# Kernel optimization log

Measured on AMD Instinct MI355X. Metric: run time of the kernel, lower is better.

Reference implementation:

```python
import jax, jax.numpy as jnp
import numpy as np
from functools import partial

GRID = 5  # 224/32 - 2
N_ANCHORS = 3
N_BOX = GRID * GRID * N_ANCHORS  # 75


def _make_anchors():
    # faithful replication of _create_anchors (grid-index cx,cy with pixel-scale w,h)
    scales = [56, 112, 224]
    a = np.zeros((GRID, GRID, N_ANCHORS, 8), np.float32)
    for x in range(GRID):
        for y in range(GRID):
            for k in range(N_ANCHORS):
                w = h = scales[k]
                a[x, y, k] = [x - w // 2, y - h // 2, x + w // 2, y + h // 2, x, y, w, h]
    return jnp.asarray(a)

ANCHORS = _make_anchors()  # [5,5,3,8]: x0,y0,x1,y1,cx,cy,w,h


def conv2d(x, w, b, pad):
    y = jax.lax.conv_general_dilated(x, w, (1, 1), [(pad, pad), (pad, pad)],
                                     dimension_numbers=('NCHW', 'OIHW', 'NCHW'))
    return y + b[None, :, None, None]


def maxpool2(x):
    return jax.lax.reduce_window(x, -jnp.inf, jax.lax.max,
                                 (1, 1, 2, 2), (1, 1, 2, 2), 'VALID')


def deparam_bboxes(rp_reg):
    # rp_reg: [B,5,5,3,4]; anchors broadcast over batch
    aw = ANCHORS[..., 6]; ah = ANCHORS[..., 7]
    ax = ANCHORS[..., 4]; ay = ANCHORS[..., 5]
    cx = rp_reg[..., 0] * aw + ax
    cy = rp_reg[..., 1] * ah + ay
    w = jnp.exp(rp_reg[..., 2]) * aw
    h = jnp.exp(rp_reg[..., 3]) * ah
    return jnp.stack([cx - w / 2, cy - h / 2, cx + w / 2, cy + h / 2], axis=-1)


def _iou_as_written(bi, bj):
    # replicates bb_intersection_over_union EXACTLY, including the missing
    # parentheses bug: inter/areaA + areaB - inter
    xA = jnp.maximum(bi[0], bj[..., 0]); yA = jnp.maximum(bi[1], bj[..., 1])
    xB = jnp.minimum(bi[2], bj[..., 2]); yB = jnp.minimum(bi[3], bj[..., 3])
    inter = jnp.maximum(0.0, xB - xA + 1) * jnp.maximum(0.0, yB - yA + 1)
    areaA = (bi[2] - bi[0] + 1) * (bi[3] - bi[1] + 1)
    areaB = (bj[..., 2] - bj[..., 0] + 1) * (bj[..., 3] - bj[..., 1] + 1)
    return inter / areaA + areaB - inter


def nms_single(boxes, scores, thresh=0.7):
    # boxes [75,4], scores [75]; greedy suppression in score order (vectorized
    # replacement of the O(n^2) Python-loop NMS in _compute_bboxes)
    order = jnp.argsort(-scores)
    b = boxes[order]
    idx = jnp.arange(N_BOX)

    def body(i, keep):
        iou = _iou_as_written(b[i], b)          # [75]
        sup = (idx > i) & (iou > thresh) & keep[i]
        return keep & ~sup

    keep_sorted = jax.lax.fori_loop(0, N_BOX, body, jnp.ones(N_BOX, bool))
    return jnp.zeros(N_BOX, bool).at[order].set(keep_sorted)


def setup_inputs() -> dict:
    key = jax.random.key(0)
    ks = jax.random.split(key, 16)
    B = 32
    inp = {"x": jax.random.normal(ks[0], (B, 3, 224, 224), jnp.float32)}
    chans = [3, 64, 128, 256, 512, 512]
    for i in range(5):
        cin, cout = chans[i], chans[i + 1]
        std = float(np.sqrt(2.0 / (cout * 9)))  # kaiming fan_out, relu
        inp[f"fw{i}"] = jax.random.normal(ks[1 + i], (cout, cin, 3, 3), jnp.float32) * std
        inp[f"fb{i}"] = jnp.zeros((cout,), jnp.float32)
    # RPN heads: normal(0, 0.01), zero bias (per _initialize_rp_weights)
    inp["rpw_w"] = jax.random.normal(ks[6], (512, 512, 3, 3), jnp.float32) * 0.01
    inp["rpw_b"] = jnp.zeros((512,), jnp.float32)
    inp["cls_w"] = jax.random.normal(ks[7], (N_ANCHORS, 512, 1, 1), jnp.float32) * 0.01
    inp["cls_b"] = jnp.zeros((N_ANCHORS,), jnp.float32)
    inp["reg_w"] = jax.random.normal(ks[8], (4 * N_ANCHORS, 512, 1, 1), jnp.float32) * 0.01
    inp["reg_b"] = jnp.zeros((4 * N_ANCHORS,), jnp.float32)
    # classifier2: Linear(512*7*7, 20), normal(0, 0.01)
    inp["fc_w"] = jax.random.normal(ks[9], (20, 512 * 7 * 7), jnp.float32) * 0.01
    inp["fc_b"] = jnp.zeros((20,), jnp.float32)
    return inp


def reference(x, fw0, fb0, fw1, fb1, fw2, fb2, fw3, fb3, fw4, fb4,
              rpw_w, rpw_b, cls_w, cls_b, reg_w, reg_b, fc_w, fc_b):
    B = x.shape[0]
    feat = x
    for w, b in ((fw0, fb0), (fw1, fb1), (fw2, fb2), (fw3, fb3), (fw4, fb4)):
        feat = maxpool2(jax.nn.relu(conv2d(feat, w, b, pad=1)))
    # feat: [B,512,7,7]
    rp512 = jax.nn.relu(conv2d(feat, rpw_w, rpw_b, pad=0))          # [B,512,5,5]
    rp_cls = jax.nn.sigmoid(conv2d(rp512, cls_w, cls_b, pad=0))     # [B,3,5,5]
    rp_reg = conv2d(rp512, reg_w, reg_b, pad=0)                     # [B,12,5,5]
    # faithful to torch .view (row-major reshape, NOT permute)
    rp_cls = rp_cls.reshape(B, GRID, GRID, N_ANCHORS)
    rp_reg = rp_reg.reshape(B, GRID, GRID, N_ANCHORS, 4)
    bboxes = deparam_bboxes(rp_reg)                                 # [B,5,5,3,4]
    keep = jax.vmap(nms_single)(bboxes.reshape(B, N_BOX, 4),
                                rp_cls.reshape(B, N_BOX))           # [B,75] bool
    logits = feat.reshape(B, -1) @ fc_w.T + fc_b                    # [B,20]
    return logits, rp_cls, rp_reg, bboxes, keep
```

## Files before the change

### kernel.cpp

```cpp
#include <hip/hip_runtime.h>
#include <math.h>


#define OFF_LOGITS 0
#define OFF_CLS    640
#define OFF_REG    3040
#define OFF_BOXES  12640
#define OFF_KEEP   22240

constexpr int BATCH = 32;

typedef _Float16 h8 __attribute__((ext_vector_type(8)));
typedef _Float16 h4 __attribute__((ext_vector_type(4)));
typedef float    f4 __attribute__((ext_vector_type(4)));

#define MFMA16(a, b, c) __builtin_amdgcn_mfma_f32_16x16x32_f16(a, b, c, 0, 0, 0)

#if defined(__has_builtin)
#  if __has_builtin(__builtin_amdgcn_global_load_lds)
#    define HAS_GLL 1
#  endif
#endif

__device__ __forceinline__ void stage16(const _Float16* g, _Float16* lbase, int lane) {
#ifdef HAS_GLL
  __builtin_amdgcn_global_load_lds((const __attribute__((address_space(1))) void*)g,
                                   (__attribute__((address_space(3))) void*)lbase,
                                   16, 0, 0);
#else
  *reinterpret_cast<h8*>(lbase + lane * 8) = *reinterpret_cast<const h8*>(g);
#endif
}

constexpr size_t A_OFF = 0;
constexpr size_t B_OFF = 106463232;
constexpr size_t W_OFF = 161579008;
constexpr size_t P_OFF = A_OFF + 8388608;

constexpr int I0_E = 26615808;
constexpr int I1_E = 13778944;
constexpr int I2_E = 7372800;
constexpr int I3_E = 4194304;
constexpr int I4_E = 802816;

__global__ __launch_bounds__(256)
void wcvt(const float* __restrict__ src, _Float16* __restrict__ dHi,
          _Float16* __restrict__ dLo, int COUT, int CIN) {
  const int total = COUT * CIN * 9;
  for (int idx = blockIdx.x * 256 + threadIdx.x; idx < total; idx += gridDim.x * 256) {
    const int co = idx / (CIN * 9);
    const int r = idx % (CIN * 9);
    const int ci = r / 9, tap = r % 9;
    const float v = src[idx];
    const _Float16 h = (_Float16)v;
    const int o = ((tap * (CIN >> 5) + (ci >> 5)) * COUT + co) * 32 + (ci & 31);
    dHi[o] = h;
    dLo[o] = (_Float16)(v - (float)h);
  }
}

__global__ __launch_bounds__(256)
void zero_ring(_Float16* __restrict__ hi, _Float16* __restrict__ lo, int P, int C) {
  const int c8n = C / 8, cells = 4 * P - 4;
  const int tot = 32 * cells * c8n;
  for (int idx = blockIdx.x * 256 + threadIdx.x; idx < tot; idx += gridDim.x * 256) {
    const int c8 = idx % c8n;
    const int cell = (idx / c8n) % cells;
    const int n = idx / (c8n * cells);
    int y, xx;
    if (cell < 2 * P) { y = (cell < P) ? 0 : (P - 1); xx = cell % P; }
    else { const int q = cell - 2 * P; y = 1 + (q >> 1); xx = (q & 1) ? (P - 1) : 0; }
    const long o = ((long)(n * P + y) * P + xx) * C + c8 * 8;
    h8 z = {};
    *reinterpret_cast<h8*>(hi + o) = z;
    *reinterpret_cast<h8*>(lo + o) = z;
  }
}

__global__ __launch_bounds__(256)
void conv_l0(const float* __restrict__ x, const float* __restrict__ w0,
             const float* __restrict__ b0, _Float16* __restrict__ outHi,
             _Float16* __restrict__ outLo) {
  const int bid = blockIdx.x;
  const int tx0 = (bid % 7) * 16, ty0 = ((bid / 7) % 7) * 16, n = bid / 49;
  __shared__ float sIn[3 * 34 * 34];
  __shared__ float sW[1728];
  __shared__ float sB[64];
  const int tid = threadIdx.x;
  for (int idx = tid; idx < 3 * 34 * 34; idx += 256) {
    const int ci = idx / 1156, rem = idx % 1156, r = rem / 34, cc = rem % 34;
    const int y = 2 * ty0 - 1 + r, xx = 2 * tx0 - 1 + cc;
    float v = 0.f;
    if ((unsigned)y < 224u && (unsigned)xx < 224u)
      v = x[((n * 3 + ci) * 224 + y) * 224 + xx];
    sIn[idx] = v;
  }
  for (int idx = tid; idx < 1728; idx += 256) sW[idx] = w0[idx];
  if (tid < 64) sB[tid] = b0[tid];
  __syncthreads();

  const int tpy = tid / 16, tpx = tid % 16;
  float win[3][4][4];
  #pragma unroll
  for (int ci = 0; ci < 3; ++ci)
    #pragma unroll
    for (int dr = 0; dr < 4; ++dr)
      #pragma unroll
      for (int dc = 0; dc < 4; ++dc)
        win[ci][dr][dc] = sIn[ci * 1156 + (2 * tpy + dr) * 34 + (2 * tpx + dc)];

  const long ob = ((long)(n * 114 + ty0 + tpy + 1) * 114 + tx0 + tpx + 1) * 64;
  for (int co4 = 0; co4 < 16; ++co4) {
    h4 hh, ll;
    #pragma unroll
    for (int j = 0; j < 4; ++j) {
      const int co = co4 * 4 + j;
      float a00 = 0.f, a01 = 0.f, a10 = 0.f, a11 = 0.f;
      #pragma unroll
      for (int ci = 0; ci < 3; ++ci)
        #pragma unroll
        for (int ky = 0; ky < 3; ++ky)
          #pragma unroll
          for (int kx = 0; kx < 3; ++kx) {
            const float wv = sW[co * 27 + ci * 9 + ky * 3 + kx];
            a00 = fmaf(win[ci][ky][kx], wv, a00);
            a01 = fmaf(win[ci][ky][kx + 1], wv, a01);
            a10 = fmaf(win[ci][ky + 1][kx], wv, a10);
            a11 = fmaf(win[ci][ky + 1][kx + 1], wv, a11);
          }
      const float p = fmaxf(fmaxf(fmaxf(a00, a01), fmaxf(a10, a11)) + sB[co], 0.f);
      const _Float16 h = (_Float16)p;
      hh[j] = h;
      ll[j] = (_Float16)(p - (float)h);
    }
    *reinterpret_cast<h4*>(outHi + ob + co4 * 4) = hh;
    *reinterpret_cast<h4*>(outLo + ob + co4 * 4) = ll;
  }
}

template<int CIN, int COUT, int H, int XPAD>
__global__ __launch_bounds__(256, 2)
void convrow(const _Float16* __restrict__ inHi, const _Float16* __restrict__ inLo,
             const _Float16* __restrict__ wHi, const _Float16* __restrict__ wLo,
             const float* __restrict__ bias, _Float16* __restrict__ outHi,
             _Float16* __restrict__ outLo) {
  constexpr int W = H, Hp = H / 2, Wp = W / 2, PW = W + 2, POW = Wp + 2;
  constexpr int BSP = XPAD * 2;
  constexpr int NSPW = BSP / 64;
  constexpr int NCOW = 4 / NSPW;
  constexpr int BCO = NCOW * 64;
  constexpr int KCH = CIN / 32;
  constexpr int NPH = 3 * KCH;
  constexpr int NISS = BSP / 64;
  __align__(16) __shared__ _Float16 sB[2][2][BSP * 32];

  const int tid = threadIdx.x;
  const int lane = tid & 63, wv = tid >> 6;
  const int c = lane & 15, kq = lane >> 4;
  const int cow = blockIdx.y * BCO + (wv % NCOW) * 64;
  const int spl = (wv / NCOW) * 64;
  const int py = blockIdx.x % Hp, n = blockIdx.x / Hp;

  int gstage[NISS];
  #pragma unroll
  for (int i = 0; i < NISS; ++i) {
    const int sl = i * 64 + tid / 4;
    const int ry = sl & 1;
    int xx = sl >> 1;
    if (xx > PW - 1) xx = PW - 1;
    gstage[i] = ((n * (H + 2) + 2 * py + ry) * PW + xx) * CIN +
                (((tid & 3) ^ ((sl >> 1) & 3)) * 8);
  }
  int dsoff[3][4];
  #pragma unroll
  for (int kx = 0; kx < 3; ++kx)
    #pragma unroll
    for (int nt = 0; nt < 4; ++nt) {
      int r = spl + nt * 16 + c + 2 * kx;
      if (r > BSP - 1) r = BSP - 1;
      dsoff[kx][nt] = r * 32 + ((kq ^ ((r >> 1) & 3)) * 8);
    }

  #pragma unroll
  for (int i = 0; i < NISS; ++i) {
    stage16(inHi + gstage[i], &sB[0][0][i * 2048 + wv * 512], lane);
    stage16(inLo + gstage[i], &sB[0][1][i * 2048 + wv * 512], lane);
  }
  __syncthreads();

  f4 acc[4][4] = {};
  int cur = 0;
  for (int ph = 0; ph < NPH; ++ph) {
    const int ky = ph / KCH, kc = ph % KCH;
    h8 aH[3][4], aL[3][4];
    #pragma unroll
    for (int kx = 0; kx < 3; ++kx) {
      const long abase = ((long)((ky * 3 + kx) * KCH + kc) * COUT + cow) * 32;
      #pragma unroll
      for (int mt = 0; mt < 4; ++mt) {
        const long ao = abase + (mt * 16 + c) * 32 + kq * 8;
        aH[kx][mt] = *reinterpret_cast<const h8*>(wHi + ao);
        aL[kx][mt] = *reinterpret_cast<const h8*>(wLo + ao);
      }
    }
    __builtin_amdgcn_sched_barrier(0);
    if (ph + 1 < NPH) {
      const int tb2 = ((ph + 1) / KCH) * PW * CIN + ((ph + 1) % KCH) * 32;
      #pragma unroll
      for (int i = 0; i < NISS; ++i) {
        stage16(inHi + gstage[i] + tb2, &sB[cur ^ 1][0][i * 2048 + wv * 512], lane);
        stage16(inLo + gstage[i] + tb2, &sB[cur ^ 1][1][i * 2048 + wv * 512], lane);
      }
    }
    __builtin_amdgcn_sched_barrier(0);
    #pragma unroll
    for (int kx = 0; kx < 3; ++kx) {
      h8 bH[4], bL[4];
      #pragma unroll
      for (int nt = 0; nt < 4; ++nt) {
        bH[nt] = *reinterpret_cast<const h8*>(&sB[cur][0][dsoff[kx][nt]]);
        bL[nt] = *reinterpret_cast<const h8*>(&sB[cur][1][dsoff[kx][nt]]);
      }
      __builtin_amdgcn_s_setprio(1);
      #pragma unroll
      for (int mt = 0; mt < 4; ++mt)
        #pragma unroll
        for (int nt = 0; nt < 4; ++nt)
          acc[mt][nt] = MFMA16(aH[kx][mt], bH[nt], acc[mt][nt]);
      #pragma unroll
      for (int mt = 0; mt < 4; ++mt)
        #pragma unroll
        for (int nt = 0; nt < 4; ++nt)
          acc[mt][nt] = MFMA16(aH[kx][mt], bL[nt], acc[mt][nt]);
      #pragma unroll
      for (int mt = 0; mt < 4; ++mt)
        #pragma unroll
        for (int nt = 0; nt < 4; ++nt)
          acc[mt][nt] = MFMA16(aL[kx][mt], bH[nt], acc[mt][nt]);
      __builtin_amdgcn_s_setprio(0);
    }
    __syncthreads();
    cur ^= 1;
  }

  const int r4 = lane >> 4;
  #pragma unroll
  for (int mt = 0; mt < 4; ++mt) {
    const int co0 = cow + mt * 16 + r4 * 4;
    const f4 bi = *reinterpret_cast<const f4*>(bias + co0);
    #pragma unroll
    for (int nt = 0; nt < 4; ++nt) {
      f4 v = acc[mt][nt];
      #pragma unroll
      for (int r = 0; r < 4; ++r) {
        const float m1 = fmaxf(v[r], __shfl_xor(v[r], 1, 64));
        v[r] = fmaxf(m1, __shfl_xor(m1, 2, 64));
      }
      if ((lane & 3) == 0) {
        const int rr = spl + nt * 16 + c;
        const int px = rr >> 2;
        if (px < Wp) {
          h4 hh, ll;
          #pragma unroll
          for (int r = 0; r < 4; ++r) {
            const float p = fmaxf(v[r] + bi[r], 0.f);
            const _Float16 h = (_Float16)p;
            hh[r] = h;
            ll[r] = (_Float16)(p - (float)h);
          }
          const long oa = ((long)((n * (Hp + 2) + py + 1) * POW + px + 1)) * COUT + co0;
          *reinterpret_cast<h4*>(outHi + oa) = hh;
          *reinterpret_cast<h4*>(outLo + oa) = ll;
        }
      }
    }
  }
}

template<int CIN, int COUT, int H, int BCO, int BSP, int TG, int KPH, int MODE>
__global__ __launch_bounds__(256, 2)
void convpool(const _Float16* __restrict__ inHi, const _Float16* __restrict__ inLo,
              const _Float16* __restrict__ wHi, const _Float16* __restrict__ wLo,
              const float* __restrict__ bias, _Float16* __restrict__ outHi,
              _Float16* __restrict__ outLo, float* __restrict__ outF) {
  constexpr int W = H, Hp = H / 2, Wp = W / 2, PW = W + 2, POW = Wp + 2;
  constexpr int NCOW = BCO / 64, NSPW = BSP / 64;
  static_assert(NCOW * NSPW == 4, "4 waves");
  constexpr int KCH = CIN / 32;
  constexpr int NCH = TG * KCH;
  constexpr int NPH = NCH / KPH;
  static_assert(NCH % KPH == 0, "even phases");
  constexpr int NISS = BSP / 64;
  constexpr int SPTOT = 32 * H * W;
  constexpr int TSZ = BSP * 32;
  __align__(16) __shared__ _Float16 sB[2 * 2 * KPH * TSZ];
  #define TIDX(buf, hl, j) ((((buf) * 2 + (hl)) * KPH + (j)) * TSZ)

  const int tid = threadIdx.x;
  const int lane = tid & 63, wv = tid >> 6;
  const int c = lane & 15, kq = lane >> 4;
  const int cow = blockIdx.y * BCO + (wv % NCOW) * 64;
  const int spl = (wv / NCOW) * 64;
  const int sblk = blockIdx.x * BSP;
  const int tap0 = (TG == 9) ? 0 : blockIdx.z * TG;

  int gstage[NISS];
  #pragma unroll
  for (int i = 0; i < NISS; ++i) {
    const int sl = i * 64 + tid / 4;
    const int sg = sblk + sl;
    const int ry = sg & 1, tt = sg >> 1;
    const int x = tt % W, u = tt / W;
    const int py = u % Hp, n = u / Hp;
    gstage[i] = ((n * (H + 2) + 2 * py + ry) * PW + x) * CIN +
                (((tid & 3) ^ ((sl >> 1) & 3)) * 8);
  }
  int dsoff[4];
  #pragma unroll
  for (int nt = 0; nt < 4; ++nt) {
    const int row = spl + nt * 16 + c;
    dsoff[nt] = row * 32 + ((kq ^ ((row >> 1) & 3)) * 8);
  }

  #pragma unroll
  for (int j = 0; j < KPH; ++j) {
    const int tap = tap0 + j / KCH, kc = j % KCH;
    const int tb = ((tap / 3) * PW + (tap % 3)) * CIN + kc * 32;
    #pragma unroll
    for (int i = 0; i < NISS; ++i) {
      stage16(inHi + gstage[i] + tb, &sB[TIDX(0, 0, j) + i * 2048 + wv * 512], lane);
      stage16(inLo + gstage[i] + tb, &sB[TIDX(0, 1, j) + i * 2048 + wv * 512], lane);
    }
  }
  __syncthreads();

  f4 acc[4][4] = {};
  int cur = 0;
  for (int ph = 0; ph < NPH; ++ph) {
    h8 aH[KPH][4], aL[KPH][4];
    #pragma unroll
    for (int j = 0; j < KPH; ++j) {
      const int ch = ph * KPH + j;
      const int tap = tap0 + ch / KCH;
      const int kc = ch % KCH;
      const long abase = ((long)(tap * KCH + kc) * COUT + cow) * 32;
      #pragma unroll
      for (int mt = 0; mt < 4; ++mt) {
        const long ao = abase + (mt * 16 + c) * 32 + kq * 8;
        aH[j][mt] = *reinterpret_cast<const h8*>(wHi + ao);
        aL[j][mt] = *reinterpret_cast<const h8*>(wLo + ao);
      }
    }
    __builtin_amdgcn_sched_barrier(0);
    if (ph + 1 < NPH) {
      #pragma unroll
      for (int j2 = 0; j2 < KPH; ++j2) {
        const int ch2 = (ph + 1) * KPH + j2;
        const int tap2 = tap0 + ch2 / KCH;
        const int tb2 = ((tap2 / 3) * PW + (tap2 % 3)) * CIN + (ch2 % KCH) * 32;
        #pragma unroll
        for (int i = 0; i < NISS; ++i) {
          stage16(inHi + gstage[i] + tb2,
                  &sB[TIDX(cur ^ 1, 0, j2) + i * 2048 + wv * 512], lane);
          stage16(inLo + gstage[i] + tb2,
                  &sB[TIDX(cur ^ 1, 1, j2) + i * 2048 + wv * 512], lane);
        }
      }
    }
    __builtin_amdgcn_sched_barrier(0);
    #pragma unroll
    for (int j = 0; j < KPH; ++j) {
      h8 bH[4], bL[4];
      #pragma unroll
      for (int nt = 0; nt < 4; ++nt) {
        bH[nt] = *reinterpret_cast<const h8*>(&sB[TIDX(cur, 0, j) + dsoff[nt]]);
        bL[nt] = *reinterpret_cast<const h8*>(&sB[TIDX(cur, 1, j) + dsoff[nt]]);
      }
      __builtin_amdgcn_s_setprio(1);
      #pragma unroll
      for (int mt = 0; mt < 4; ++mt)
        #pragma unroll
        for (int nt = 0; nt < 4; ++nt)
          acc[mt][nt] = MFMA16(aH[j][mt], bH[nt], acc[mt][nt]);
      #pragma unroll
      for (int mt = 0; mt < 4; ++mt)
        #pragma unroll
        for (int nt = 0; nt < 4; ++nt)
          acc[mt][nt] = MFMA16(aH[j][mt], bL[nt], acc[mt][nt]);
      #pragma unroll
      for (int mt = 0; mt < 4; ++mt)
        #pragma unroll
        for (int nt = 0; nt < 4; ++nt)
          acc[mt][nt] = MFMA16(aL[j][mt], bH[nt], acc[mt][nt]);
      __builtin_amdgcn_s_setprio(0);
    }
    __syncthreads();
    cur ^= 1;
  }
  #undef TIDX

  const int r4 = lane >> 4;
  if (MODE == 1) {
    #pragma unroll
    for (int mt = 0; mt < 4; ++mt) {
      const int co0 = cow + mt * 16 + r4 * 4;
      #pragma unroll
      for (int nt = 0; nt < 4; ++nt) {
        const int s = sblk + spl + nt * 16 + c;
        *reinterpret_cast<f4*>(outF + ((long)blockIdx.z * SPTOT + s) * COUT + co0) =
            acc[mt][nt];
      }
    }
  } else {
    #pragma unroll
    for (int mt = 0; mt < 4; ++mt) {
      const int co0 = cow + mt * 16 + r4 * 4;
      const f4 bi = *reinterpret_cast<const f4*>(bias + co0);
      #pragma unroll
      for (int nt = 0; nt < 4; ++nt) {
        f4 v = acc[mt][nt];
        #pragma unroll
        for (int r = 0; r < 4; ++r) {
          const float m1 = fmaxf(v[r], __shfl_xor(v[r], 1, 64));
          v[r] = fmaxf(m1, __shfl_xor(m1, 2, 64));
        }
        if ((lane & 3) == 0) {
          const int s = sblk + spl + nt * 16 + c;
          const int ps = s >> 2;
          const int n = ps / (Hp * Wp), rem = ps % (Hp * Wp);
          const int py = rem / Wp, px = rem % Wp;
          h4 hh, ll;
          #pragma unroll
          for (int r = 0; r < 4; ++r) {
            const float p = fmaxf(v[r] + bi[r], 0.f);
            const _Float16 h = (_Float16)p;
            hh[r] = h;
            ll[r] = (_Float16)(p - (float)h);
          }
          const long oa = ((long)((n * (Hp + 2) + py + 1) * POW + px + 1)) * COUT + co0;
          *reinterpret_cast<h4*>(outHi + oa) = hh;
          *reinterpret_cast<h4*>(outLo + oa) = ll;
        }
      }
    }
  }
}

__global__ __launch_bounds__(256)
void l4_finish(const float* __restrict__ part, const float* __restrict__ bias,
               _Float16* __restrict__ I4h, _Float16* __restrict__ I4l,
               float* __restrict__ feat) {
  const int t = blockIdx.x * 256 + threadIdx.x;
  if (t >= 1568 * 128) return;
  const int co0 = (t % 128) * 4, p = t / 128;
  f4 m;
  #pragma unroll
  for (int q = 0; q < 4; ++q) {
    const long s = 4L * p + q;
    f4 v = *reinterpret_cast<const f4*>(part + s * 512 + co0);
    v += *reinterpret_cast<const f4*>(part + (6272 + s) * 512 + co0);
    v += *reinterpret_cast<const f4*>(part + (12544 + s) * 512 + co0);
    if (q == 0) m = v;
    else {
      #pragma unroll
      for (int r = 0; r < 4; ++r) m[r] = fmaxf(m[r], v[r]);
    }
  }
  const f4 bi = *reinterpret_cast<const f4*>(bias + co0);
  h4 hh, ll;
  const int n = p / 49, pix = p % 49;
  #pragma unroll
  for (int r = 0; r < 4; ++r) {
    const float pv = fmaxf(m[r] + bi[r], 0.f);
    const _Float16 h = (_Float16)pv;
    hh[r] = h;
    ll[r] = (_Float16)(pv - (float)h);
    feat[((long)(n * 512 + co0 + r)) * 49 + pix] = pv;
  }
  *reinterpret_cast<h4*>(I4h + (long)p * 512 + co0) = hh;
  *reinterpret_cast<h4*>(I4l + (long)p * 512 + co0) = ll;
}

__global__ __launch_bounds__(256)
void rpn_partial(const _Float16* __restrict__ inHi, const _Float16* __restrict__ inLo,
                 const _Float16* __restrict__ wHi, const _Float16* __restrict__ wLo,
                 float* __restrict__ part) {
  const int lane = threadIdx.x & 63, wv = threadIdx.x >> 6;
  const int cow = blockIdx.y * 128 + wv * 32;
  const int sblk = blockIdx.x * 64;
  const int tap = blockIdx.z, ky = tap / 3, kx = tap % 3;
  const int c = lane & 15, kq = lane >> 4;

  int baseB[4];
  #pragma unroll
  for (int nt = 0; nt < 4; ++nt) {
    int s = sblk + nt * 16 + c;
    if (s > 799) s = 799;
    const int n = s / 25, pix = s % 25, py = pix / 5, px = pix % 5;
    baseB[nt] = ((n * 7 + py + ky) * 7 + px + kx) * 512;
  }

  f4 acc[2][4] = {};
  for (int kch = 0; kch < 16; ++kch) {
    h8 aH[2], aL[2], bH[4], bL[4];
    const long abase = ((long)(tap * 16 + kch) * 512 + cow) * 32;
    #pragma unroll
    for (int mt = 0; mt < 2; ++mt) {
      const long ao = abase + (mt * 16 + c) * 32 + kq * 8;
      aH[mt] = *reinterpret_cast<const h8*>(wHi + ao);
      aL[mt] = *reinterpret_cast<const h8*>(wLo + ao);
    }
    #pragma unroll
    for (int nt = 0; nt < 4; ++nt) {
      const int bo = baseB[nt] + kch * 32 + kq * 8;
      bH[nt] = *reinterpret_cast<const h8*>(inHi + bo);
      bL[nt] = *reinterpret_cast<const h8*>(inLo + bo);
    }
    #pragma unroll
    for (int mt = 0; mt < 2; ++mt)
      #pragma unroll
      for (int nt = 0; nt < 4; ++nt)
        acc[mt][nt] = MFMA16(aH[mt], bH[nt], acc[mt][nt]);
    #pragma unroll
    for (int mt = 0; mt < 2; ++mt)
      #pragma unroll
      for (int nt = 0; nt < 4; ++nt)
        acc[mt][nt] = MFMA16(aH[mt], bL[nt], acc[mt][nt]);
    #pragma unroll
    for (int mt = 0; mt < 2; ++mt)
      #pragma unroll
      for (int nt = 0; nt < 4; ++nt)
        acc[mt][nt] = MFMA16(aL[mt], bH[nt], acc[mt][nt]);
  }

  const int r4 = lane >> 4;
  #pragma unroll
  for (int mt = 0; mt < 2; ++mt) {
    const int co0 = cow + mt * 16 + r4 * 4;
    #pragma unroll
    for (int nt = 0; nt < 4; ++nt) {
      const int s = sblk + nt * 16 + c;
      if (s < 800)
        *reinterpret_cast<f4*>(part + ((long)tap * 800 + s) * 512 + co0) = acc[mt][nt];
    }
  }
}

__global__ __launch_bounds__(256)
void rpn_finish(const float* __restrict__ part, const float* __restrict__ bias,
                float* __restrict__ rp512) {
  const int t = blockIdx.x * 256 + threadIdx.x;
  if (t >= 800 * 128) return;
  const int co0 = (t % 128) * 4, s = t / 128;
  f4 acc = *reinterpret_cast<const f4*>(bias + co0);
  #pragma unroll
  for (int g = 0; g < 9; ++g)
    acc += *reinterpret_cast<const f4*>(part + ((long)g * 800 + s) * 512 + co0);
  f4 o;
  #pragma unroll
  for (int r = 0; r < 4; ++r) o[r] = fmaxf(acc[r], 0.f);
  *reinterpret_cast<f4*>(rp512 + (long)s * 512 + co0) = o;
}

__global__ __launch_bounds__(256)
void heads_kernel(const float* __restrict__ rp512,
                  const float* __restrict__ cls_w, const float* __restrict__ cls_b,
                  const float* __restrict__ reg_w, const float* __restrict__ reg_b,
                  float* __restrict__ out) {
  const int idx = blockIdx.x * 256 + threadIdx.x;
  if (idx >= 32 * 25 * 15) return;
  const int o = idx % 15, pix = (idx / 15) % 25, n = idx / 375;
  const float* __restrict__ ip = rp512 + ((long)(n * 25 + pix)) * 512;
  const float* __restrict__ wvp = (o < 3) ? (cls_w + o * 512) : (reg_w + (o - 3) * 512);
  float acc = 0.f;
  for (int k = 0; k < 512; k += 4) {
    const f4 a = *reinterpret_cast<const f4*>(ip + k);
    const f4 b = *reinterpret_cast<const f4*>(wvp + k);
    acc = fmaf(a[0], b[0], acc); acc = fmaf(a[1], b[1], acc);
    acc = fmaf(a[2], b[2], acc); acc = fmaf(a[3], b[3], acc);
  }
  if (o < 3) {
    acc += cls_b[o];
    out[OFF_CLS + n * 75 + o * 25 + pix] = 1.f / (1.f + expf(-acc));
  } else {
    acc += reg_b[o - 3];
    out[OFF_REG + n * 300 + (o - 3) * 25 + pix] = acc;
  }
}

__global__ __launch_bounds__(256)
void fc_kernel(const float* __restrict__ feat, const float* __restrict__ fw,
               const float* __restrict__ fb, float* __restrict__ out) {
  const int n = blockIdx.x, j = blockIdx.y;
  const float* __restrict__ ip = feat + (long)n * 25088;
  const float* __restrict__ wj = fw + (long)j * 25088;
  float acc = 0.f;
  for (int k = threadIdx.x * 4; k < 25088; k += 1024) {
    const f4 a = *reinterpret_cast<const f4*>(ip + k);
    const f4 b = *reinterpret_cast<const f4*>(wj + k);
    acc = fmaf(a[0], b[0], acc); acc = fmaf(a[1], b[1], acc);
    acc = fmaf(a[2], b[2], acc); acc = fmaf(a[3], b[3], acc);
  }
  #pragma unroll
  for (int m = 32; m >= 1; m >>= 1) acc += __shfl_xor(acc, m, 64);
  __shared__ float red[4];
  const int wv = threadIdx.x >> 6;
  if ((threadIdx.x & 63) == 0) red[wv] = acc;
  __syncthreads();
  if (threadIdx.x == 0)
    out[OFF_LOGITS + n * 20 + j] = red[0] + red[1] + red[2] + red[3] + fb[j];
}

__global__ __launch_bounds__(128)
void bbox_nms_kernel(float* __restrict__ out) {
  const int n = blockIdx.x;
  const int t = threadIdx.x;
  __shared__ float bx0[75], by0[75], bx1[75], by1[75], area[75], sc[75];
  __shared__ int rank_s[75], order_s[75], keep_s[75];

  if (t < 75) {
    const int g1 = t / 15, g2 = (t / 3) % 5, a = t % 3;
    const float aw = (a == 0) ? 56.f : (a == 1 ? 112.f : 224.f);
    const float r0 = out[OFF_REG + n * 300 + 4 * t + 0];
    const float r1 = out[OFF_REG + n * 300 + 4 * t + 1];
    const float r2 = out[OFF_REG + n * 300 + 4 * t + 2];
    const float r3 = out[OFF_REG + n * 300 + 4 * t + 3];
    const float cx = r0 * aw + (float)g1;
    const float cy = r1 * aw + (float)g2;
    const float w_ = expf(r2) * aw;
    const float h_ = expf(r3) * aw;
    const float x0 = cx - 0.5f * w_, y0 = cy - 0.5f * h_;
    const float x1 = cx + 0.5f * w_, y1 = cy + 0.5f * h_;
    bx0[t] = x0; by0[t] = y0; bx1[t] = x1; by1[t] = y1;
    area[t] = (x1 - x0 + 1.f) * (y1 - y0 + 1.f);
    out[OFF_BOXES + n * 300 + 4 * t + 0] = x0;
    out[OFF_BOXES + n * 300 + 4 * t + 1] = y0;
    out[OFF_BOXES + n * 300 + 4 * t + 2] = x1;
    out[OFF_BOXES + n * 300 + 4 * t + 3] = y1;
    sc[t] = out[OFF_CLS + n * 75 + t];
    keep_s[t] = 1;
  }
  __syncthreads();
  if (t < 75) {
    const float si = sc[t];
    int rk = 0;
    for (int j = 0; j < 75; ++j) {
      const float sj = sc[j];
      rk += (sj > si) || (sj == si && j < t);
    }
    rank_s[t] = rk;
    order_s[rk] = t;
  }
  __syncthreads();
  for (int i = 0; i < 74; ++i) {
    if (keep_s[i]) {
      const int bi = order_s[i];
      if (t > i && t < 75) {
        const int bj = order_s[t];
        const float xA = fmaxf(bx0[bi], bx0[bj]);
        const float yA = fmaxf(by0[bi], by0[bj]);
        const float xB = fminf(bx1[bi], bx1[bj]);
        const float yB = fminf(by1[bi], by1[bj]);
        const float inter = fmaxf(0.f, xB - xA + 1.f) * fmaxf(0.f, yB - yA + 1.f);
        const float iou = inter / area[bi] + area[bj] - inter;
        if (iou > 0.7f) keep_s[t] = 0;
      }
    }
    __syncthreads();
  }
  if (t < 75) out[OFF_KEEP + n * 75 + t] = keep_s[rank_s[t]] ? 1.f : 0.f;
}

extern "C" void kernel_launch(void* const* d_in, const int* in_sizes, int n_in,
                              void* d_out, int out_size, void* d_ws, size_t ws_size,
                              hipStream_t stream) {
  (void)in_sizes; (void)n_in; (void)out_size; (void)ws_size;
  const float* x     = (const float*)d_in[0];
  const float* fw0   = (const float*)d_in[1];
  const float* fb0   = (const float*)d_in[2];
  const float* fw1   = (const float*)d_in[3];
  const float* fb1   = (const float*)d_in[4];
  const float* fw2   = (const float*)d_in[5];
  const float* fb2   = (const float*)d_in[6];
  const float* fw3   = (const float*)d_in[7];
  const float* fb3   = (const float*)d_in[8];
  const float* fw4   = (const float*)d_in[9];
  const float* fb4   = (const float*)d_in[10];
  const float* rpw_w = (const float*)d_in[11];
  const float* rpw_b = (const float*)d_in[12];
  const float* cls_w = (const float*)d_in[13];
  const float* cls_b = (const float*)d_in[14];
  const float* reg_w = (const float*)d_in[15];
  const float* reg_b = (const float*)d_in[16];
  const float* fc_w  = (const float*)d_in[17];
  const float* fc_b  = (const float*)d_in[18];
  float* out = (float*)d_out;
  char* ws = (char*)d_ws;

  _Float16* I0h = (_Float16*)(ws + A_OFF);
  _Float16* I0l = I0h + I0_E;
  _Float16* I1h = (_Float16*)(ws + B_OFF);
  _Float16* I1l = I1h + I1_E;
  _Float16* I2h = (_Float16*)(ws + A_OFF);
  _Float16* I2l = I2h + I2_E;
  _Float16* I3h = (_Float16*)(ws + B_OFF);
  _Float16* I3l = I3h + I3_E;
  _Float16* I4h = (_Float16*)(ws + A_OFF);
  _Float16* I4l = I4h + I4_E;
  float* feat  = (float*)(ws + A_OFF + (size_t)I4_E * 4);
  float* rp512 = (float*)(ws + A_OFF + (size_t)I4_E * 4 + 3211264);
  float* part  = (float*)(ws + P_OFF);

  _Float16* w1h = (_Float16*)(ws + W_OFF);                _Float16* w1l = w1h + 73728;
  _Float16* w2h = (_Float16*)(ws + W_OFF + 294912);       _Float16* w2l = w2h + 294912;
  _Float16* w3h = (_Float16*)(ws + W_OFF + 1474560);      _Float16* w3l = w3h + 1179648;
  _Float16* w4h = (_Float16*)(ws + W_OFF + 6193152);      _Float16* w4l = w4h + 2359296;
  _Float16* wrh = (_Float16*)(ws + W_OFF + 15630336);     _Float16* wrl = wrh + 2359296;

  wcvt<<<(73728 + 255) / 256, 256, 0, stream>>>(fw1, w1h, w1l, 128, 64);
  wcvt<<<(294912 + 255) / 256, 256, 0, stream>>>(fw2, w2h, w2l, 256, 128);
  wcvt<<<(1179648 + 255) / 256, 256, 0, stream>>>(fw3, w3h, w3l, 512, 256);
  wcvt<<<(2359296 + 255) / 256, 256, 0, stream>>>(fw4, w4h, w4l, 512, 512);
  wcvt<<<(2359296 + 255) / 256, 256, 0, stream>>>(rpw_w, wrh, wrl, 512, 512);

  zero_ring<<<512, 256, 0, stream>>>(I0h, I0l, 114, 64);
  zero_ring<<<512, 256, 0, stream>>>(I1h, I1l, 58, 128);

  conv_l0<<<32 * 49, 256, 0, stream>>>(x, fw0, fb0, I0h, I0l);

  convrow<64, 128, 112, 128><<<dim3(32 * 56, 2), 256, 0, stream>>>(
      I0h, I0l, w1h, w1l, fb1, I1h, I1l);
  zero_ring<<<512, 256, 0, stream>>>(I2h, I2l, 30, 256);
  convrow<128, 256, 56, 64><<<dim3(32 * 28, 2), 256, 0, stream>>>(
      I1h, I1l, w2h, w2l, fb2, I2h, I2l);
  zero_ring<<<512, 256, 0, stream>>>(I3h, I3l, 16, 512);
  convrow<256, 512, 28, 32><<<dim3(32 * 14, 2), 256, 0, stream>>>(
      I2h, I2l, w3h, w3l, fb3, I3h, I3l);
  convpool<512, 512, 14, 256, 64, 3, 2, 1><<<dim3(98, 2, 3), 256, 0, stream>>>(
      I3h, I3l, w4h, w4l, nullptr, nullptr, nullptr, part);
  l4_finish<<<(1568 * 128 + 255) / 256, 256, 0, stream>>>(part, fb4, I4h, I4l, feat);

  rpn_partial<<<dim3(13, 4, 9), 256, 0, stream>>>(I4h, I4l, wrh, wrl, part);
  rpn_finish<<<(800 * 128 + 255) / 256, 256, 0, stream>>>(part, rpw_b, rp512);

  heads_kernel<<<(12000 + 255) / 256, 256, 0, stream>>>(rp512, cls_w, cls_b, reg_w, reg_b, out);
  fc_kernel<<<dim3(32, 20), 256, 0, stream>>>(feat, fc_w, fc_b, out);
  bbox_nms_kernel<<<BATCH, 128, 0, stream>>>(out);
}
```

Measured before the change: 1.023 ms.

## Retile conv layers, triple-buffer convpool staging, and coalesce layer-0 output stores

Layer 0 now stages its fp16 hi/lo outputs in shared memory and writes them back as 16-byte coalesced stores instead of strided 8-byte ones. Layer 1 moves to a new convrow2 that splits each output row into 64-pixel halves with a fixed 128-channel tile per block. Layers 2 and 3 switch from the row kernel to the convpool implicit-GEMM kernel. convpool moves from double to triple buffering: it prefetches two phases ahead, uses a partial vmcnt wait and raw s_barrier, and no longer waits for all loads each phase. The aim is more latency hiding and better grid occupancy, at the cost of more LDS per block and a fragile hand-written waitcnt assumption.

```diff
diff --git a/kernel.cpp b/kernel.cpp
--- a/kernel.cpp
+++ b/kernel.cpp
@@ -77,15 +77,23 @@
   }
 }
 
+constexpr int L0_SW   = 0;
+constexpr int L0_SB   = 6912;
+constexpr int L0_SIN  = 7168;
+constexpr int L0_HI   = 7168;
+constexpr int L0_LO   = 7168 + 36864;
+constexpr int L0_LDS  = 7168 + 73728;
+
 __global__ __launch_bounds__(256)
 void conv_l0(const float* __restrict__ x, const float* __restrict__ w0,
              const float* __restrict__ b0, _Float16* __restrict__ outHi,
              _Float16* __restrict__ outLo) {
   const int bid = blockIdx.x;
   const int tx0 = (bid % 7) * 16, ty0 = ((bid / 7) % 7) * 16, n = bid / 49;
-  __shared__ float sIn[3 * 34 * 34];
-  __shared__ float sW[1728];
-  __shared__ float sB[64];
+  __align__(16) __shared__ char lds[L0_LDS];
+  float* sW = (float*)(lds + L0_SW);
+  float* sB = (float*)(lds + L0_SB);
+  float* sIn = (float*)(lds + L0_SIN);
   const int tid = threadIdx.x;
   for (int idx = tid; idx < 3 * 34 * 34; idx += 256) {
     const int ci = idx / 1156, rem = idx % 1156, r = rem / 34, cc = rem % 34;
@@ -108,8 +116,8 @@
       #pragma unroll
       for (int dc = 0; dc < 4; ++dc)
         win[ci][dr][dc] = sIn[ci * 1156 + (2 * tpy + dr) * 34 + (2 * tpx + dc)];
-
-  const long ob = ((long)(n * 114 + ty0 + tpy + 1) * 114 + tx0 + tpx + 1) * 64;
+  __syncthreads();
+
   for (int co4 = 0; co4 < 16; ++co4) {
     h4 hh, ll;
     #pragma unroll
@@ -133,40 +141,55 @@
       hh[j] = h;
       ll[j] = (_Float16)(p - (float)h);
     }
-    *reinterpret_cast<h4*>(outHi + ob + co4 * 4) = hh;
-    *reinterpret_cast<h4*>(outLo + ob + co4 * 4) = ll;
-  }
-}
-
-template<int CIN, int COUT, int H, int XPAD>
+    *reinterpret_cast<h4*>(lds + L0_HI + tid * 144 + co4 * 8) = hh;
+    *reinterpret_cast<h4*>(lds + L0_LO + tid * 144 + co4 * 8) = ll;
+  }
+  __syncthreads();
+
+  const int tr_half = tid >> 7;
+  const int pixrow = (tid & 127) >> 3;
+  const int ch8 = (tid & 7) * 8;
+  #pragma unroll
+  for (int i = 0; i < 8; ++i) {
+    const int tr = 2 * i + tr_half;
+    const int pix = tr * 16 + pixrow;
+    const long ga = ((long)(n * 114 + ty0 + tr + 1) * 114 + tx0 + pixrow + 1) * 64 + ch8;
+    *reinterpret_cast<h8*>(outHi + ga) =
+        *reinterpret_cast<const h8*>(lds + L0_HI + pix * 144 + ch8 * 2);
+    *reinterpret_cast<h8*>(outLo + ga) =
+        *reinterpret_cast<const h8*>(lds + L0_LO + pix * 144 + ch8 * 2);
+  }
+}
+
+template<int CIN, int COUT, int H>
 __global__ __launch_bounds__(256, 2)
-void convrow(const _Float16* __restrict__ inHi, const _Float16* __restrict__ inLo,
-             const _Float16* __restrict__ wHi, const _Float16* __restrict__ wLo,
-             const float* __restrict__ bias, _Float16* __restrict__ outHi,
-             _Float16* __restrict__ outLo) {
+void convrow2(const _Float16* __restrict__ inHi, const _Float16* __restrict__ inLo,
+              const _Float16* __restrict__ wHi, const _Float16* __restrict__ wLo,
+              const float* __restrict__ bias, _Float16* __restrict__ outHi,
+              _Float16* __restrict__ outLo) {
   constexpr int W = H, Hp = H / 2, Wp = W / 2, PW = W + 2, POW = Wp + 2;
-  constexpr int BSP = XPAD * 2;
-  constexpr int NSPW = BSP / 64;
-  constexpr int NCOW = 4 / NSPW;
-  constexpr int BCO = NCOW * 64;
   constexpr int KCH = CIN / 32;
   constexpr int NPH = 3 * KCH;
-  constexpr int NISS = BSP / 64;
-  __align__(16) __shared__ _Float16 sB[2][2][BSP * 32];
+  constexpr int STG = 136;
+  constexpr int XH = (W + 63) / 64;
+  __align__(16) __shared__ _Float16 sB[2][2][STG * 32];
 
   const int tid = threadIdx.x;
   const int lane = tid & 63, wv = tid >> 6;
   const int c = lane & 15, kq = lane >> 4;
-  const int cow = blockIdx.y * BCO + (wv % NCOW) * 64;
-  const int spl = (wv / NCOW) * 64;
-  const int py = blockIdx.x % Hp, n = blockIdx.x / Hp;
-
-  int gstage[NISS];
-  #pragma unroll
-  for (int i = 0; i < NISS; ++i) {
+  const int cow = (wv & 1) * 64;
+  const int spl = (wv >> 1) * 64;
+  const int xh = blockIdx.x % XH;
+  const int pyn = blockIdx.x / XH;
+  const int py = pyn % Hp, n = pyn / Hp;
+  const int x0 = xh * 64;
+
+  int gstage[3];
+  #pragma unroll
+  for (int i = 0; i < 3; ++i) {
     const int sl = i * 64 + tid / 4;
     const int ry = sl & 1;
-    int xx = sl >> 1;
+    int xx = x0 + (sl >> 1);
     if (xx > PW - 1) xx = PW - 1;
     gstage[i] = ((n * (H + 2) + 2 * py + ry) * PW + xx) * CIN +
                 (((tid & 3) ^ ((sl >> 1) & 3)) * 8);
@@ -176,15 +199,18 @@
   for (int kx = 0; kx < 3; ++kx)
     #pragma unroll
     for (int nt = 0; nt < 4; ++nt) {
-      int r = spl + nt * 16 + c + 2 * kx;
-      if (r > BSP - 1) r = BSP - 1;
+      const int r = spl + nt * 16 + c + 2 * kx;
       dsoff[kx][nt] = r * 32 + ((kq ^ ((r >> 1) & 3)) * 8);
     }
 
   #pragma unroll
-  for (int i = 0; i < NISS; ++i) {
+  for (int i = 0; i < 2; ++i) {
     stage16(inHi + gstage[i], &sB[0][0][i * 2048 + wv * 512], lane);
     stage16(inLo + gstage[i], &sB[0][1][i * 2048 + wv * 512], lane);
+  }
+  if (tid < 16) {
+    stage16(inHi + gstage[2], &sB[0][0][4096], lane);
+    stage16(inLo + gstage[2], &sB[0][1][4096], lane);
   }
   __syncthreads();
 
@@ -192,29 +218,28 @@
   int cur = 0;
   for (int ph = 0; ph < NPH; ++ph) {
     const int ky = ph / KCH, kc = ph % KCH;
-    h8 aH[3][4], aL[3][4];
+    if (ph + 1 < NPH) {
+      const int tb2 = ((ph + 1) / KCH) * PW * CIN + ((ph + 1) % KCH) * 32;
+      #pragma unroll
+      for (int i = 0; i < 2; ++i) {
+        stage16(inHi + gstage[i] + tb2, &sB[cur ^ 1][0][i * 2048 + wv * 512], lane);
+        stage16(inLo + gstage[i] + tb2, &sB[cur ^ 1][1][i * 2048 + wv * 512], lane);
+      }
+      if (tid < 16) {
+        stage16(inHi + gstage[2] + tb2, &sB[cur ^ 1][0][4096], lane);
+        stage16(inLo + gstage[2] + tb2, &sB[cur ^ 1][1][4096], lane);
+      }
+    }
     #pragma unroll
     for (int kx = 0; kx < 3; ++kx) {
+      h8 aH[4], aL[4];
       const long abase = ((long)((ky * 3 + kx) * KCH + kc) * COUT + cow) * 32;
       #pragma unroll
       for (int mt = 0; mt < 4; ++mt) {
         const long ao = abase + (mt * 16 + c) * 32 + kq * 8;
-        aH[kx][mt] = *reinterpret_cast<const h8*>(wHi + ao);
-        aL[kx][mt] = *reinterpret_cast<const h8*>(wLo + ao);
-      }
-    }
-    __builtin_amdgcn_sched_barrier(0);
-    if (ph + 1 < NPH) {
-      const int tb2 = ((ph + 1) / KCH) * PW * CIN + ((ph + 1) % KCH) * 32;
-      #pragma unroll
-      for (int i = 0; i < NISS; ++i) {
-        stage16(inHi + gstage[i] + tb2, &sB[cur ^ 1][0][i * 2048 + wv * 512], lane);
-        stage16(inLo + gstage[i] + tb2, &sB[cur ^ 1][1][i * 2048 + wv * 512], lane);
-      }
-    }
-    __builtin_amdgcn_sched_barrier(0);
-    #pragma unroll
-    for (int kx = 0; kx < 3; ++kx) {
+        aH[mt] = *reinterpret_cast<const h8*>(wHi + ao);
+        aL[mt] = *reinterpret_cast<const h8*>(wLo + ao);
+      }
       h8 bH[4], bL[4];
       #pragma unroll
       for (int nt = 0; nt < 4; ++nt) {
@@ -226,17 +251,17 @@
       for (int mt = 0; mt < 4; ++mt)
         #pragma unroll
         for (int nt = 0; nt < 4; ++nt)
-          acc[mt][nt] = MFMA16(aH[kx][mt], bH[nt], acc[mt][nt]);
+          acc[mt][nt] = MFMA16(aH[mt], bH[nt], acc[mt][nt]);
       #pragma unroll
       for (int mt = 0; mt < 4; ++mt)
         #pragma unroll
         for (int nt = 0; nt < 4; ++nt)
-          acc[mt][nt] = MFMA16(aH[kx][mt], bL[nt], acc[mt][nt]);
+          acc[mt][nt] = MFMA16(aH[mt], bL[nt], acc[mt][nt]);
       #pragma unroll
       for (int mt = 0; mt < 4; ++mt)
         #pragma unroll
         for (int nt = 0; nt < 4; ++nt)
-          acc[mt][nt] = MFMA16(aL[kx][mt], bH[nt], acc[mt][nt]);
+          acc[mt][nt] = MFMA16(aL[mt], bH[nt], acc[mt][nt]);
       __builtin_amdgcn_s_setprio(0);
     }
     __syncthreads();
@@ -258,8 +283,8 @@
       }
       if ((lane & 3) == 0) {
         const int rr = spl + nt * 16 + c;
-        const int px = rr >> 2;
-        if (px < Wp) {
+        const int pxg = xh * 32 + (rr >> 2);
+        if (pxg < Wp) {
           h4 hh, ll;
           #pragma unroll
           for (int r = 0; r < 4; ++r) {
@@ -268,7 +293,7 @@
             hh[r] = h;
             ll[r] = (_Float16)(p - (float)h);
           }
-          const long oa = ((long)((n * (Hp + 2) + py + 1) * POW + px + 1)) * COUT + co0;
+          const long oa = ((long)((n * (Hp + 2) + py + 1) * POW + pxg + 1)) * COUT + co0;
           *reinterpret_cast<h4*>(outHi + oa) = hh;
           *reinterpret_cast<h4*>(outLo + oa) = ll;
         }
@@ -290,10 +315,11 @@
   constexpr int NCH = TG * KCH;
   constexpr int NPH = NCH / KPH;
   static_assert(NCH % KPH == 0, "even phases");
+  static_assert(KPH * 2 * (BSP / 64) == 4, "prologue vmcnt literal = 4");
   constexpr int NISS = BSP / 64;
   constexpr int SPTOT = 32 * H * W;
   constexpr int TSZ = BSP * 32;
-  __align__(16) __shared__ _Float16 sB[2 * 2 * KPH * TSZ];
+  __align__(16) __shared__ _Float16 sB[3 * 2 * KPH * TSZ];
   #define TIDX(buf, hl, j) ((((buf) * 2 + (hl)) * KPH + (j)) * TSZ)
 
   const int tid = threadIdx.x;
@@ -323,20 +349,28 @@
   }
 
   #pragma unroll
-  for (int j = 0; j < KPH; ++j) {
-    const int tap = tap0 + j / KCH, kc = j % KCH;
-    const int tb = ((tap / 3) * PW + (tap % 3)) * CIN + kc * 32;
-    #pragma unroll
-    for (int i = 0; i < NISS; ++i) {
-      stage16(inHi + gstage[i] + tb, &sB[TIDX(0, 0, j) + i * 2048 + wv * 512], lane);
-      stage16(inLo + gstage[i] + tb, &sB[TIDX(0, 1, j) + i * 2048 + wv * 512], lane);
-    }
-  }
-  __syncthreads();
+  for (int pp = 0; pp < 2; ++pp) {
+    #pragma unroll
+    for (int j = 0; j < KPH; ++j) {
+      const int ch = pp * KPH + j;
+      const int tap = tap0 + ch / KCH, kc = ch % KCH;
+      const int tb = ((tap / 3) * PW + (tap % 3)) * CIN + kc * 32;
+      #pragma unroll
+      for (int i = 0; i < NISS; ++i) {
+        stage16(inHi + gstage[i] + tb, &sB[TIDX(pp, 0, j) + i * 2048 + wv * 512], lane);
+        stage16(inLo + gstage[i] + tb, &sB[TIDX(pp, 1, j) + i * 2048 + wv * 512], lane);
+      }
+    }
+  }
+  __builtin_amdgcn_sched_barrier(0);
+  asm volatile("s_waitcnt vmcnt(4)" ::: "memory");
+  __builtin_amdgcn_sched_barrier(0);
+  __builtin_amdgcn_s_barrier();
+  __builtin_amdgcn_sched_barrier(0);
 
   f4 acc[4][4] = {};
-  int cur = 0;
   for (int ph = 0; ph < NPH; ++ph) {
+    const int bp = ph % 3;
     h8 aH[KPH][4], aL[KPH][4];
     #pragma unroll
     for (int j = 0; j < KPH; ++j) {
@@ -352,18 +386,19 @@
       }
     }
     __builtin_amdgcn_sched_barrier(0);
-    if (ph + 1 < NPH) {
+    if (ph + 2 < NPH) {
+      const int bs = (ph + 2) % 3;
       #pragma unroll
       for (int j2 = 0; j2 < KPH; ++j2) {
-        const int ch2 = (ph + 1) * KPH + j2;
+        const int ch2 = (ph + 2) * KPH + j2;
         const int tap2 = tap0 + ch2 / KCH;
         const int tb2 = ((tap2 / 3) * PW + (tap2 % 3)) * CIN + (ch2 % KCH) * 32;
         #pragma unroll
         for (int i = 0; i < NISS; ++i) {
           stage16(inHi + gstage[i] + tb2,
-                  &sB[TIDX(cur ^ 1, 0, j2) + i * 2048 + wv * 512], lane);
+                  &sB[TIDX(bs, 0, j2) + i * 2048 + wv * 512], lane);
           stage16(inLo + gstage[i] + tb2,
-                  &sB[TIDX(cur ^ 1, 1, j2) + i * 2048 + wv * 512], lane);
+                  &sB[TIDX(bs, 1, j2) + i * 2048 + wv * 512], lane);
         }
       }
     }
@@ -373,8 +408,8 @@
       h8 bH[4], bL[4];
       #pragma unroll
       for (int nt = 0; nt < 4; ++nt) {
-        bH[nt] = *reinterpret_cast<const h8*>(&sB[TIDX(cur, 0, j) + dsoff[nt]]);
-        bL[nt] = *reinterpret_cast<const h8*>(&sB[TIDX(cur, 1, j) + dsoff[nt]]);
+        bH[nt] = *reinterpret_cast<const h8*>(&sB[TIDX(bp, 0, j) + dsoff[nt]]);
+        bL[nt] = *reinterpret_cast<const h8*>(&sB[TIDX(bp, 1, j) + dsoff[nt]]);
       }
       __builtin_amdgcn_s_setprio(1);
       #pragma unroll
@@ -394,8 +429,9 @@
           acc[mt][nt] = MFMA16(aL[j][mt], bH[nt], acc[mt][nt]);
       __builtin_amdgcn_s_setprio(0);
     }
-    __syncthreads();
-    cur ^= 1;
+    __builtin_amdgcn_sched_barrier(0);
+    __builtin_amdgcn_s_barrier();
+    __builtin_amdgcn_sched_barrier(0);
   }
   #undef TIDX
 
@@ -728,14 +764,14 @@
 
   conv_l0<<<32 * 49, 256, 0, stream>>>(x, fw0, fb0, I0h, I0l);
 
-  convrow<64, 128, 112, 128><<<dim3(32 * 56, 2), 256, 0, stream>>>(
+  convrow2<64, 128, 112><<<dim3(32 * 56 * 2, 1, 1), 256, 0, stream>>>(
       I0h, I0l, w1h, w1l, fb1, I1h, I1l);
   zero_ring<<<512, 256, 0, stream>>>(I2h, I2l, 30, 256);
-  convrow<128, 256, 56, 64><<<dim3(32 * 28, 2), 256, 0, stream>>>(
-      I1h, I1l, w2h, w2l, fb2, I2h, I2l);
+  convpool<128, 256, 56, 256, 64, 9, 2, 0><<<dim3(1568, 1, 1), 256, 0, stream>>>(
+      I1h, I1l, w2h, w2l, fb2, I2h, I2l, nullptr);
   zero_ring<<<512, 256, 0, stream>>>(I3h, I3l, 16, 512);
-  convrow<256, 512, 28, 32><<<dim3(32 * 14, 2), 256, 0, stream>>>(
-      I2h, I2l, w3h, w3l, fb3, I3h, I3l);
+  convpool<256, 512, 28, 256, 64, 9, 2, 0><<<dim3(392, 2, 1), 256, 0, stream>>>(
+      I2h, I2l, w3h, w3l, fb3, I3h, I3l, nullptr);
   convpool<512, 512, 14, 256, 64, 3, 2, 1><<<dim3(98, 2, 3), 256, 0, stream>>>(
       I3h, I3l, w4h, w4l, nullptr, nullptr, nullptr, part);
   l4_finish<<<(1568 * 128 + 255) / 256, 256, 0, stream>>>(part, fb4, I4h, I4l, feat);
```

Result: faster. 884.2 us (-13.6%).
